# Performance work log

Hardware: AMD Instinct MI355X
Metric: run time of the kernel (lower is better)

## Reference

```python
import jax, jax.numpy as jnp
import numpy as np

B, S, H = 8, 2048, 1024

def setup_inputs() -> dict:
    key = jax.random.key(0)
    k1, k2, k3, k4, k5, k6 = jax.random.split(key, 6)
    scale = 1.0 / np.sqrt(H)
    return {
        "hidden_states": jax.random.normal(k1, (B, S, H), dtype=jnp.float32),
        "key_padding_mask": jax.random.bernoulli(k2, 0.1, (B, S)),  # True = padded key
        "Wq_w": jax.random.normal(k3, (H, H), dtype=jnp.float32) * scale,
        "Wq_b": jax.random.normal(k4, (H,), dtype=jnp.float32) * 0.01,
        "Wk_w": jax.random.normal(k5, (H, H), dtype=jnp.float32) * scale,
        "Wk_b": jax.random.normal(k6, (H,), dtype=jnp.float32) * 0.01,
    }

def reference(hidden_states, key_padding_mask, Wq_w, Wq_b, Wk_w, Wk_b):
    # torch nn.Linear: y = x @ W.T + b
    q = jnp.einsum("bsh,oh->bso", hidden_states, Wq_w) + Wq_b
    k = jnp.einsum("bsh,oh->bso", hidden_states, Wk_w) + Wk_b
    d = q.shape[-1]
    scores = jnp.einsum("bqd,bkd->bqk", q, k) / jnp.sqrt(jnp.asarray(d, q.dtype))
    # scores[mask] -= inf  -> masked key columns become -inf
    scores = jnp.where(key_padding_mask[:, None, :], -jnp.inf, scores)
    attn = jax.nn.softmax(scores, axis=2)  # [B, S, S]
    out = jnp.einsum("bqk,bkd->bqd", attn, hidden_states)  # values = hidden_states (no proj)
    return out
```

## Files before the change

### kernel.cpp

```cpp
#include <hip/hip_runtime.h>
#include <hip/hip_bf16.h>

using bf16 = __hip_bfloat16;

using frag_ab = __attribute__((ext_vector_type(8))) short;
using frag_cd = __attribute__((ext_vector_type(4))) float;

#define TM 128
#define TN 128
#define TK 32

__device__ __forceinline__ unsigned short f2bu(float f) {
    bf16 h = __float2bfloat16(f);
    return *(unsigned short*)&h;
}

__device__ __forceinline__ void st_c(float* p, float v) { *p = v; }
__device__ __forceinline__ void st_c(bf16* p, float v)  { *p = __float2bfloat16(v); }

__device__ __forceinline__ void load16(const bf16* g, bf16* l) {
    __builtin_amdgcn_global_load_lds(
        (const __attribute__((address_space(1))) unsigned int*)g,
        (__attribute__((address_space(3))) unsigned int*)l,
        16, 0, 0);
}

#define WAIT_VM4()  __builtin_amdgcn_s_waitcnt(0x0F74)
#define FENCE()     __asm__ __volatile__("" ::: "memory")

template <typename TC, bool HAS_BIAS, bool MASK>
__global__ __launch_bounds__(256, 4)
void mfma_gemm_nt(const bf16* __restrict__ A, const bf16* __restrict__ B,
                  const float* __restrict__ bias, const int* __restrict__ mask,
                  TC* __restrict__ C, int N, int K, int lda, int ldb, int ldc,
                  long sA, long sB, long sC, long sM, float scale)
{
    __shared__ bf16 As[3][TM][TK];
    __shared__ bf16 Bs[3][TN][TK];

    const int bz = blockIdx.z;
    const bf16* Ab = A + (long)bz * sA;
    const bf16* Bb = B + (long)bz * sB;
    TC* Cb = C + (long)bz * sC;
    const int* maskb = MASK ? (mask + (long)bz * sM) : nullptr;

    const int t  = threadIdx.x;
    const int m0 = blockIdx.x * TM;
    const int n0 = blockIdx.y * TN;

    const int srow = t >> 2;
    const int c    = t & 3;
    const int gco  = (((c - (srow >> 1)) & 3) << 3);
    const int lco  = c << 3;
    const bf16* ga0 = Ab + (long)(m0 + srow) * lda + gco;
    const bf16* ga1 = ga0 + (long)64 * lda;
    const bf16* gb0 = Bb + (long)(n0 + srow) * ldb + gco;
    const bf16* gb1 = gb0 + (long)64 * ldb;

    const int wave = t >> 6;
    const int lane = t & 63;
    const int wm   = (wave & 1) * 64;
    const int wn   = (wave >> 1) * 64;
    const int lrow = lane & 15;
    const int quad = lane >> 4;
    const int rco  = (((quad + (lrow >> 1)) & 3) << 3);

    frag_cd acc[4][4] = {};

#define STAGE(buf)                                         \
    do {                                                   \
        load16(ga0, &As[buf][srow][lco]);                  \
        load16(ga1, &As[buf][srow + 64][lco]);             \
        load16(gb0, &Bs[buf][srow][lco]);                  \
        load16(gb1, &Bs[buf][srow + 64][lco]);             \
        ga0 += TK; ga1 += TK; gb0 += TK; gb1 += TK;        \
    } while (0)

    const int nIt = K / TK;
    STAGE(0);
    STAGE(1);

    int cur = 0, nxt = 2;
    for (int it = 0; it < nIt; ++it) {
        WAIT_VM4();
        FENCE();
        __builtin_amdgcn_s_barrier();
        FENCE();

        if (it + 2 < nIt) {
            STAGE(nxt);
            nxt = (nxt == 2) ? 0 : nxt + 1;
        }

        frag_ab af[4], bfv[4];
#pragma unroll
        for (int i = 0; i < 4; ++i)
            af[i] = *(const frag_ab*)&As[cur][wm + i * 16 + lrow][rco];
#pragma unroll
        for (int j = 0; j < 4; ++j)
            bfv[j] = *(const frag_ab*)&Bs[cur][wn + j * 16 + lrow][rco];
#pragma unroll
        for (int i = 0; i < 4; ++i)
#pragma unroll
            for (int j = 0; j < 4; ++j)
                acc[i][j] = __builtin_amdgcn_mfma_f32_16x16x32_bf16(
                    af[i], bfv[j], acc[i][j], 0, 0, 0);

        cur = (cur == 2) ? 0 : cur + 1;
    }
#undef STAGE

#pragma unroll
    for (int j = 0; j < 4; ++j) {
        const int col = n0 + wn + j * 16 + lrow;
        const float bv = HAS_BIAS ? bias[col] : 0.0f;
        const bool msk = MASK ? (maskb[col] != 0) : false;
#pragma unroll
        for (int i = 0; i < 4; ++i) {
            const int rbase = m0 + wm + i * 16 + quad * 4;
#pragma unroll
            for (int r = 0; r < 4; ++r) {
                float v = acc[i][j][r] * scale + bv;
                if (MASK && msk) v = -INFINITY;
                st_c(&Cb[(long)(rbase + r) * ldc + col], v);
            }
        }
    }
}

__global__ __launch_bounds__(256)
void convert_transpose(const float* __restrict__ X, bf16* __restrict__ Xb,
                       bf16* __restrict__ XT, int S, int H)
{
    __shared__ unsigned short tile[64][72];
    const int b = blockIdx.z;
    const float* Xp = X + (long)b * S * H;
    bf16* Xbp = Xb + (long)b * S * H;
    bf16* XTp = XT + (long)b * H * S;
    const int h0 = blockIdx.x * 64, s0 = blockIdx.y * 64;
    const int t = threadIdx.x;
    const int r  = t >> 4;
    const int c4 = (t & 15) * 4;

#pragma unroll
    for (int p = 0; p < 4; ++p) {
        const int row = r + p * 16;
        const float4 v = *(const float4*)&Xp[(long)(s0 + row) * H + h0 + c4];
        ushort4 u;
        u.x = f2bu(v.x); u.y = f2bu(v.y); u.z = f2bu(v.z); u.w = f2bu(v.w);
        *(ushort4*)&tile[row][c4] = u;
        *(ushort4*)&Xbp[(long)(s0 + row) * H + h0 + c4] = u;
    }
    __syncthreads();
#pragma unroll
    for (int p = 0; p < 4; ++p) {
        const int hrow = r + p * 16;
        ushort4 u;
        u.x = tile[c4 + 0][hrow];
        u.y = tile[c4 + 1][hrow];
        u.z = tile[c4 + 2][hrow];
        u.w = tile[c4 + 3][hrow];
        *(ushort4*)&XTp[(long)(h0 + hrow) * S + s0 + c4] = u;
    }
}

__global__ __launch_bounds__(256)
void convert_w2(const float* __restrict__ wa, const float* __restrict__ wb,
                bf16* __restrict__ out, int n4each,
                const float* __restrict__ qb, const float* __restrict__ kb,
                float* __restrict__ biasP, int H)
{
    const int blk = blockIdx.x;
    if (blk == 2 * n4each / 256) {
        for (int i = threadIdx.x; i < 2 * H; i += 256)
            biasP[i] = (i < H) ? qb[i] : kb[i - H];
        return;
    }
    const int i = blk * 256 + threadIdx.x;
    const bool second = i >= n4each;
    const float* src = second ? wb : wa;
    const int j = second ? i - n4each : i;
    const float4 v = ((const float4*)src)[j];
    ushort4 u;
    u.x = f2bu(v.x); u.y = f2bu(v.y); u.z = f2bu(v.z); u.w = f2bu(v.w);
    ((ushort4*)out)[i] = u;
}

__global__ __launch_bounds__(256)
void softmax_kernel(bf16* __restrict__ Smat, int Slen)
{
    const int row = blockIdx.x;
    bf16* srow = Smat + (long)row * Slen;

    const int t    = threadIdx.x;
    const int lane = t & 63;
    const int wid  = t >> 6;

    ushort4 u0 = ((const ushort4*)srow)[t * 2];
    ushort4 u1 = ((const ushort4*)srow)[t * 2 + 1];

    float vals[8];
    {
        const unsigned short us[8] = {u0.x, u0.y, u0.z, u0.w, u1.x, u1.y, u1.z, u1.w};
#pragma unroll
        for (int i = 0; i < 8; ++i) {
            unsigned int w = (unsigned int)us[i] << 16;
            vals[i] = *(float*)&w;
        }
    }

    float mx = vals[0];
#pragma unroll
    for (int i = 1; i < 8; ++i) mx = fmaxf(mx, vals[i]);

    __shared__ float red[4];
#pragma unroll
    for (int o = 32; o > 0; o >>= 1) mx = fmaxf(mx, __shfl_xor(mx, o, 64));
    if (lane == 0) red[wid] = mx;
    __syncthreads();
    mx = fmaxf(fmaxf(red[0], red[1]), fmaxf(red[2], red[3]));
    __syncthreads();

    float sum = 0.0f;
#pragma unroll
    for (int i = 0; i < 8; ++i) {
        const float e = __expf(vals[i] - mx);
        vals[i] = e;
        sum += e;
    }
#pragma unroll
    for (int o = 32; o > 0; o >>= 1) sum += __shfl_xor(sum, o, 64);
    if (lane == 0) red[wid] = sum;
    __syncthreads();
    sum = red[0] + red[1] + red[2] + red[3];

    const float inv = 1.0f / sum;
    ushort4 o0, o1;
    o0.x = f2bu(vals[0] * inv); o0.y = f2bu(vals[1] * inv);
    o0.z = f2bu(vals[2] * inv); o0.w = f2bu(vals[3] * inv);
    o1.x = f2bu(vals[4] * inv); o1.y = f2bu(vals[5] * inv);
    o1.z = f2bu(vals[6] * inv); o1.w = f2bu(vals[7] * inv);
    ((ushort4*)srow)[t * 2]     = o0;
    ((ushort4*)srow)[t * 2 + 1] = o1;
}

extern "C" void kernel_launch(void* const* d_in, const int* in_sizes, int n_in,
                              void* d_out, int out_size, void* d_ws, size_t ws_size,
                              hipStream_t stream)
{
    const float* hidden = (const float*)d_in[0];
    const int*   mask   = (const int*)d_in[1];
    const float* Wq_w   = (const float*)d_in[2];
    const float* Wq_b   = (const float*)d_in[3];
    const float* Wk_w   = (const float*)d_in[4];
    const float* Wk_b   = (const float*)d_in[5];
    float* out = (float*)d_out;

    const int B = 8, S = 2048, H = 1024;
    const int M = B * S;
    const long MH = (long)M * H;

    bf16* QK  = (bf16*)d_ws;
    bf16* XbT = QK + MH * 2;
    bf16* Sb  = XbT + MH;
    bf16* Xb  = Sb;
    bf16* Wb  = Xb + MH;
    float* biasP = (float*)(Wb + 2L * H * H);

    const dim3 blk(256);

    convert_transpose<<<dim3(H / 64, S / 64, B), blk, 0, stream>>>(hidden, Xb, XbT, S, H);
    convert_w2<<<dim3(2 * H * H / 1024 + 1), blk, 0, stream>>>(
        Wq_w, Wk_w, Wb, H * H / 4, Wq_b, Wk_b, biasP, H);

    mfma_gemm_nt<bf16, true, false><<<dim3(M / TM, 2 * H / TN, 1), blk, 0, stream>>>(
        Xb, Wb, biasP, nullptr, QK, 2 * H, H, H, H, 2 * H, 0, 0, 0, 0, 1.0f);

    mfma_gemm_nt<bf16, false, true><<<dim3(S / TM, S / TN, B), blk, 0, stream>>>(
        QK, QK + H, nullptr, mask, Sb, S, H, 2 * H, 2 * H, S,
        (long)S * 2 * H, (long)S * 2 * H, (long)S * S, S, 1.0f / 32.0f);

    softmax_kernel<<<dim3(B * S), blk, 0, stream>>>(Sb, S);

    mfma_gemm_nt<float, false, false><<<dim3(S / TM, H / TN, B), blk, 0, stream>>>(
        Sb, XbT, nullptr, nullptr, out, H, S, S, S, H,
        (long)S * S, (long)H * S, (long)S * H, 0, 1.0f);
}
```

Baseline: 441.1 us.

## Load B fragments directly from global to registers, double-buffer only A in LDS

The B operand tile no longer goes through shared memory. Each wave loads its B MFMA fragments straight from global memory into registers, prefetched one K-step ahead. The A tile pipeline drops from triple to double buffering with a plain __syncthreads per iteration, which cuts LDS use and may allow more occupancy. In exchange, B rows are re-read by the two waves that share the same wn, the global B loads are strided per lane (less coalesced), and the prefetch is only one stage deep.

```diff
diff --git a/kernel.cpp b/kernel.cpp
--- a/kernel.cpp
+++ b/kernel.cpp
@@ -24,9 +24,6 @@
         (__attribute__((address_space(3))) unsigned int*)l,
         16, 0, 0);
 }
-
-#define WAIT_VM4()  __builtin_amdgcn_s_waitcnt(0x0F74)
-#define FENCE()     __asm__ __volatile__("" ::: "memory")
 
 template <typename TC, bool HAS_BIAS, bool MASK>
 __global__ __launch_bounds__(256, 4)
@@ -35,8 +32,7 @@
                   TC* __restrict__ C, int N, int K, int lda, int ldb, int ldc,
                   long sA, long sB, long sC, long sM, float scale)
 {
-    __shared__ bf16 As[3][TM][TK];
-    __shared__ bf16 Bs[3][TN][TK];
+    __shared__ bf16 As[2][TM][TK];
 
     const int bz = blockIdx.z;
     const bf16* Ab = A + (long)bz * sA;
@@ -54,8 +50,6 @@
     const int lco  = c << 3;
     const bf16* ga0 = Ab + (long)(m0 + srow) * lda + gco;
     const bf16* ga1 = ga0 + (long)64 * lda;
-    const bf16* gb0 = Bb + (long)(n0 + srow) * ldb + gco;
-    const bf16* gb1 = gb0 + (long)64 * ldb;
 
     const int wave = t >> 6;
     const int lane = t & 63;
@@ -65,50 +59,54 @@
     const int quad = lane >> 4;
     const int rco  = (((quad + (lrow >> 1)) & 3) << 3);
 
+    const bf16* gb[4];
+#pragma unroll
+    for (int j = 0; j < 4; ++j)
+        gb[j] = Bb + (long)(n0 + wn + j * 16 + lrow) * ldb + (quad << 3);
+
     frag_cd acc[4][4] = {};
-
-#define STAGE(buf)                                         \
-    do {                                                   \
-        load16(ga0, &As[buf][srow][lco]);                  \
-        load16(ga1, &As[buf][srow + 64][lco]);             \
-        load16(gb0, &Bs[buf][srow][lco]);                  \
-        load16(gb1, &Bs[buf][srow + 64][lco]);             \
-        ga0 += TK; ga1 += TK; gb0 += TK; gb1 += TK;        \
+    frag_ab bc[4], bn[4];
+
+#define STAGE_A(buf)                                   \
+    do {                                               \
+        load16(ga0, &As[buf][srow][lco]);              \
+        load16(ga1, &As[buf][srow + 64][lco]);         \
+        ga0 += TK; ga1 += TK;                          \
     } while (0)
 
-    const int nIt = K / TK;
-    STAGE(0);
-    STAGE(1);
-
-    int cur = 0, nxt = 2;
-    for (int it = 0; it < nIt; ++it) {
-        WAIT_VM4();
-        FENCE();
-        __builtin_amdgcn_s_barrier();
-        FENCE();
-
-        if (it + 2 < nIt) {
-            STAGE(nxt);
-            nxt = (nxt == 2) ? 0 : nxt + 1;
+#pragma unroll
+    for (int j = 0; j < 4; ++j) { bc[j] = *(const frag_ab*)gb[j]; gb[j] += TK; }
+    STAGE_A(0);
+    __syncthreads();
+
+#pragma unroll
+    for (int j = 0; j < 4; ++j) bn[j] = bc[j];
+
+    int cur = 0;
+    for (int k0 = 0; k0 < K; k0 += TK) {
+        if (k0 + TK < K) {
+#pragma unroll
+            for (int j = 0; j < 4; ++j) { bn[j] = *(const frag_ab*)gb[j]; gb[j] += TK; }
+            STAGE_A(cur ^ 1);
         }
 
-        frag_ab af[4], bfv[4];
+        frag_ab af[4];
 #pragma unroll
         for (int i = 0; i < 4; ++i)
             af[i] = *(const frag_ab*)&As[cur][wm + i * 16 + lrow][rco];
 #pragma unroll
-        for (int j = 0; j < 4; ++j)
-            bfv[j] = *(const frag_ab*)&Bs[cur][wn + j * 16 + lrow][rco];
-#pragma unroll
         for (int i = 0; i < 4; ++i)
 #pragma unroll
             for (int j = 0; j < 4; ++j)
                 acc[i][j] = __builtin_amdgcn_mfma_f32_16x16x32_bf16(
-                    af[i], bfv[j], acc[i][j], 0, 0, 0);
-
-        cur = (cur == 2) ? 0 : cur + 1;
-    }
-#undef STAGE
+                    af[i], bc[j], acc[i][j], 0, 0, 0);
+
+        __syncthreads();
+#pragma unroll
+        for (int j = 0; j < 4; ++j) bc[j] = bn[j];
+        cur ^= 1;
+    }
+#undef STAGE_A
 
 #pragma unroll
     for (int j = 0; j < 4; ++j) {
```

Measured after the change: 589.6 us. 33.7% more time.
